# Kernel optimization log

Measured on AMD Instinct MI355X. Metric: run time of the kernel, lower is better.

The kernel has to match this reference:

```python
import jax, jax.numpy as jnp
import numpy as np

N = 100000   # nodes
E = 3200000  # edges
D = 256      # node_dim
H = 64       # hidden (conv1 out)
L = 64       # latent_dim
G = 128      # graphs in batch


def _gcn_conv(x, src, dst, W, b):
    """PyG GCNConv with edge_weight=1: add self-loops, sym deg-norm, scatter-add."""
    n = x.shape[0]
    loop = jnp.arange(n)
    s = jnp.concatenate([src, loop])
    d = jnp.concatenate([dst, loop])
    w = jnp.ones(s.shape[0], x.dtype)
    deg = jax.ops.segment_sum(w, d, num_segments=n)
    dinv = jnp.where(deg > 0, jax.lax.rsqrt(deg), 0.0)
    norm = dinv[s] * w * dinv[d]                      # [E+N]
    h = x @ W                                         # lin (no bias)
    out = jax.ops.segment_sum(h[s] * norm[:, None], d, num_segments=n)
    return out + b


def _mean_pool(z, batch, num_graphs):
    zsum = jax.ops.segment_sum(z, batch, num_segments=num_graphs)
    cnt = jax.ops.segment_sum(jnp.ones(z.shape[0], z.dtype), batch, num_segments=num_graphs)
    return zsum / jnp.clip(cnt, 1.0)[:, None]


def setup_inputs() -> dict:
    key = jax.random.key(0)
    ks = jax.random.split(key, 8)
    x = jax.random.normal(ks[0], (N, D), jnp.float32)
    edge_index = jax.random.randint(ks[1], (2, E), 0, N, dtype=jnp.int64)
    batch = jnp.sort(jax.random.randint(ks[2], (N,), 0, G, dtype=jnp.int64))
    glorot = lambda k, fi, fo: jax.random.normal(k, (fi, fo), jnp.float32) / np.sqrt(fi).astype(np.float32)
    return {
        "x": x, "edge_index": edge_index, "batch": batch,
        "W1": glorot(ks[3], D, H), "b1": jnp.zeros((H,), jnp.float32),
        "W2": glorot(ks[4], H, L), "b2": jnp.zeros((L,), jnp.float32),
        "Wd1": glorot(ks[5], L, 64), "bd1": jnp.zeros((64,), jnp.float32),
        "Wd2": glorot(ks[6], 64, D), "bd2": jnp.zeros((D,), jnp.float32),
    }


def reference(x, edge_index, batch, W1, b1, W2, b2, Wd1, bd1, Wd2, bd2):
    src, dst = edge_index[0], edge_index[1]
    h = jax.nn.relu(_gcn_conv(x, src, dst, W1, b1))
    z = _gcn_conv(h, src, dst, W2, b2)
    z_pool = _mean_pool(z, batch, G)                  # [G, L]
    x_hat = jax.nn.relu(z_pool @ Wd1 + bd1) @ Wd2 + bd2  # [G, D]
    return (x_hat, z_pool)
```

## Files before the change

kernel.cpp:

```cpp
#include <hip/hip_runtime.h>
#include <hip/hip_bf16.h>
#include <hip/hip_fp16.h>
#include <hip/hip_fp8.h>

namespace {
constexpr int kN = 100000;
constexpr int kE = 3200000;
constexpr int kD = 256;
constexpr int kH = 64;
constexpr int kG = 128;

constexpr int kNB   = 782;
constexpr int kCapS = 4608;
constexpr int kCap  = 64;
constexpr int kNPad = 100352;

constexpr size_t kSlBytes = (size_t)(kN + 1) * 32;

constexpr size_t kAlign = 512;
constexpr size_t align_up(size_t v) { return (v + kAlign - 1) & ~(kAlign - 1); }

constexpr size_t OFF_CURD = 0;
constexpr size_t OFF_GCNT = OFF_CURD + align_up(kNB * 4);
constexpr size_t OFF_QRAW = OFF_GCNT + kAlign;
constexpr size_t ZERO_BYTES = OFF_QRAW + align_up((size_t)kG * kH * 4);
constexpr size_t OFF_CNT  = ZERO_BYTES;
constexpr size_t OFF_DINV = OFF_CNT + align_up((size_t)kNPad * 4);
constexpr size_t OFF_SD   = OFF_DINV + align_up((size_t)kNPad * 4);
constexpr size_t OFF_REC  = OFF_SD + align_up((size_t)kNB * kCapS * 4);
constexpr size_t OFF_HL   = OFF_REC + align_up((size_t)kNPad * kCap * 4);
constexpr size_t OFF_H2   = OFF_HL + align_up((size_t)(kN + 1) * kH);
}

__device__ __forceinline__ unsigned pack4_fp8(float a, float b, float c, float d) {
#if __has_builtin(__builtin_amdgcn_cvt_pk_fp8_f32)
    int r = 0;
    r = __builtin_amdgcn_cvt_pk_fp8_f32(a, b, r, false);
    r = __builtin_amdgcn_cvt_pk_fp8_f32(c, d, r, true);
    return (unsigned)r;
#else
    __hip_fp8_e4m3 qa(a), qb(b), qc(c), qd(d);
    return (unsigned)qa.__x | ((unsigned)qb.__x << 8)
         | ((unsigned)qc.__x << 16) | ((unsigned)qd.__x << 24);
#endif
}

__device__ __forceinline__ void add4q(float (&acc)[4], unsigned u) {
#if __has_builtin(__builtin_amdgcn_cvt_pk_f32_fp8)
    typedef float v2f __attribute__((ext_vector_type(2)));
    v2f f0 = __builtin_amdgcn_cvt_pk_f32_fp8((int)u, false);
    v2f f1 = __builtin_amdgcn_cvt_pk_f32_fp8((int)u, true);
    acc[0] += f0.x; acc[1] += f0.y; acc[2] += f1.x; acc[3] += f1.y;
#else
    #pragma unroll
    for (int j = 0; j < 4; ++j) {
        __hip_fp8_e4m3 v; v.__x = (__hip_fp8_storage_t)((u >> (8 * j)) & 0xFF);
        acc[j] += (float)v;
    }
#endif
}

__device__ __forceinline__ void add8q(float (&acc)[8], uint2 u) {
    float* a0 = acc;
    float* a1 = acc + 4;
    add4q(*(float(*)[4])a0, u.x);
    add4q(*(float(*)[4])a1, u.y);
}

__global__ __launch_bounds__(1024) void k_bucket(const int* __restrict__ src,
                                                 const int* __restrict__ dst,
                                                 int* __restrict__ curD,
                                                 unsigned* __restrict__ streamD) {
    __shared__ int cD[kNB], bD[kNB];
    int t = threadIdx.x;
    for (int i = t; i < kNB; i += 1024) cD[i] = 0;
    __syncthreads();
    int e0 = blockIdx.x * 16384;
    #pragma unroll
    for (int k = 0; k < 16; ++k) {
        int e = e0 + k * 1024 + t;
        if (e < kE) atomicAdd(&cD[dst[e] >> 7], 1);
    }
    __syncthreads();
    for (int i = t; i < kNB; i += 1024)
        bD[i] = cD[i] ? atomicAdd(&curD[i], cD[i]) : 0;
    __syncthreads();
    for (int i = t; i < kNB; i += 1024) cD[i] = 0;
    __syncthreads();
    #pragma unroll
    for (int k = 0; k < 16; ++k) {
        int e = e0 + k * 1024 + t;
        if (e < kE) {
            int s = src[e], d = dst[e];
            int pd = bD[d >> 7] + atomicAdd(&cD[d >> 7], 1);
            if (pd < kCapS)
                streamD[(size_t)(d >> 7) * kCapS + pd] =
                    ((unsigned)(d & 127) << 17) | (unsigned)s;
        }
    }
}

__global__ __launch_bounds__(256) void k_fillB(const int* __restrict__ curD,
                                               const unsigned* __restrict__ streamD,
                                               int* __restrict__ rec,
                                               int* __restrict__ cnt) {
    __shared__ int lc[128];
    int b = blockIdx.x, t = threadIdx.x;
    if (t < 128) lc[t] = 0;
    __syncthreads();
    int n = min(curD[b], kCapS);
    const unsigned* sp = streamD + (size_t)b * kCapS;
    for (int i = t; i < n; i += 256) {
        unsigned u = sp[i];
        int dlo = (u >> 17) & 127;
        int slot = atomicAdd(&lc[dlo], 1);
        if (slot < kCap)
            rec[((((size_t)b << 7) | dlo) << 6) + slot] = (int)(u & 0x1FFFF);
    }
    __syncthreads();
    if (t < 128) {
        int d = (b << 7) + t;
        if (d < kNPad) cnt[d] = lc[t];
    }
}

__global__ void k_gcnt(const int* __restrict__ batch, int* __restrict__ gcnt) {
    __shared__ int h[kG];
    int t = threadIdx.x;
    if (t < kG) h[t] = 0;
    __syncthreads();
    for (int i = blockIdx.x * blockDim.x + t; i < kN; i += gridDim.x * blockDim.x)
        atomicAdd(&h[batch[i]], 1);
    __syncthreads();
    if (t < kG && h[t]) atomicAdd(&gcnt[t], h[t]);
}

__global__ void k_dinv(const int* __restrict__ cnt, float* __restrict__ dinv,
                       unsigned* __restrict__ hl8, unsigned* __restrict__ h8) {
    int i = blockIdx.x * blockDim.x + threadIdx.x;
    if (i < kN) dinv[i] = rsqrtf((float)(cnt[i] + 1));
    if (blockIdx.x == 0 && threadIdx.x < 32) {
        int t = threadIdx.x;
        if (t < 16) {
            hl8[(size_t)kN * 16 + t] = 0u;
        } else {
            int s = (t >> 3) & 1;
            int j = t & 7;
            h8[(s * kSlBytes) / 4 + (size_t)kN * 8 + j] = 0u;
        }
    }
}

__global__ __launch_bounds__(256) void k_gemm1(const float* __restrict__ x,
                                               const float* __restrict__ W1,
                                               const float* __restrict__ dinv,
                                               unsigned char* __restrict__ hl8) {
    constexpr int TM = 64;
    constexpr int KC = 32;
    __shared__ float xs[KC][TM + 4];
    __shared__ float ws[KC][kH];
    int t = threadIdx.x;
    int tx = t & 15;
    int ty = t >> 4;
    int nb = blockIdx.x * TM;
    float acc[4][4] = {};
    for (int k0 = 0; k0 < kD; k0 += KC) {
        #pragma unroll
        for (int j = 0; j < 2; ++j) {
            int id = t * 2 + j;
            int row = id >> 3;
            int c4 = (id & 7) * 4;
            int node = nb + row;
            if (node >= kN) node = kN - 1;
            float4 v = *(const float4*)(x + (size_t)node * kD + k0 + c4);
            xs[c4 + 0][row] = v.x;
            xs[c4 + 1][row] = v.y;
            xs[c4 + 2][row] = v.z;
            xs[c4 + 3][row] = v.w;
        }
        #pragma unroll
        for (int j = 0; j < 2; ++j) {
            int id = t * 2 + j;
            int row = id >> 4;
            int c4 = (id & 15) * 4;
            float4 v = *(const float4*)(W1 + (size_t)(k0 + row) * kH + c4);
            *(float4*)&ws[row][c4] = v;
        }
        __syncthreads();
        #pragma unroll
        for (int kk = 0; kk < KC; ++kk) {
            float4 a = *(const float4*)&xs[kk][ty * 4];
            float4 b = *(const float4*)&ws[kk][tx * 4];
            acc[0][0] = fmaf(a.x, b.x, acc[0][0]); acc[0][1] = fmaf(a.x, b.y, acc[0][1]);
            acc[0][2] = fmaf(a.x, b.z, acc[0][2]); acc[0][3] = fmaf(a.x, b.w, acc[0][3]);
            acc[1][0] = fmaf(a.y, b.x, acc[1][0]); acc[1][1] = fmaf(a.y, b.y, acc[1][1]);
            acc[1][2] = fmaf(a.y, b.z, acc[1][2]); acc[1][3] = fmaf(a.y, b.w, acc[1][3]);
            acc[2][0] = fmaf(a.z, b.x, acc[2][0]); acc[2][1] = fmaf(a.z, b.y, acc[2][1]);
            acc[2][2] = fmaf(a.z, b.z, acc[2][2]); acc[2][3] = fmaf(a.z, b.w, acc[2][3]);
            acc[3][0] = fmaf(a.w, b.x, acc[3][0]); acc[3][1] = fmaf(a.w, b.y, acc[3][1]);
            acc[3][2] = fmaf(a.w, b.z, acc[3][2]); acc[3][3] = fmaf(a.w, b.w, acc[3][3]);
        }
        __syncthreads();
    }
    #pragma unroll
    for (int i = 0; i < 4; ++i) {
        int node = nb + ty * 4 + i;
        if (node < kN) {
            float di = dinv[node];
            unsigned p = pack4_fp8(di * acc[i][0], di * acc[i][1],
                                   di * acc[i][2], di * acc[i][3]);
            *(unsigned*)(hl8 + (size_t)node * kH + tx * 4) = p;
        }
    }
}

__global__ __launch_bounds__(256) void k_conv1(const int* __restrict__ rec,
                                               const int* __restrict__ cnt,
                                               const float* __restrict__ dinv,
                                               const unsigned char* __restrict__ hl8,
                                               const float* __restrict__ b1,
                                               unsigned char* __restrict__ h8) {
    int tid = threadIdx.x;
    int lane = tid & 63;
    int node = blockIdx.x * 4 + (tid >> 6);
    if (node >= kN) return;
    int slot = lane >> 3;
    int fl = lane & 7;
    size_t base = (size_t)node << 6;
    int len = min(cnt[node], kCap);
    float acc0[8] = {}, acc1[8] = {};
    for (int c0 = 0; c0 < len; c0 += 16) {
        int e0 = c0 + slot;
        int e1 = c0 + 8 + slot;
        int s0 = (e0 < len) ? rec[base + e0] : kN;
        int s1 = (e1 < len) ? rec[base + e1] : kN;
        uint2 v0 = *(const uint2*)(hl8 + ((size_t)s0 << 6) + fl * 8);
        uint2 v1 = *(const uint2*)(hl8 + ((size_t)s1 << 6) + fl * 8);
        add8q(acc0, v0);
        add8q(acc1, v1);
    }
    #pragma unroll
    for (int j = 0; j < 8; ++j) acc0[j] += acc1[j];
    #pragma unroll
    for (int d = 8; d < 64; d <<= 1) {
        #pragma unroll
        for (int j = 0; j < 8; ++j) acc0[j] += __shfl_xor(acc0[j], d, 64);
    }
    if (slot == 0) {
        uint2 sv = *(const uint2*)(hl8 + ((size_t)node << 6) + fl * 8);
        add8q(acc0, sv);
        float di = dinv[node];
        float4 ba = *(const float4*)(b1 + fl * 8);
        float4 bb = *(const float4*)(b1 + fl * 8 + 4);
        float bz[8] = {ba.x, ba.y, ba.z, ba.w, bb.x, bb.y, bb.z, bb.w};
        float r[8];
        #pragma unroll
        for (int j = 0; j < 8; ++j)
            r[j] = di * fmaxf(fmaf(di, acc0[j], bz[j]), 0.f);
        uint2 o;
        o.x = pack4_fp8(r[0], r[1], r[2], r[3]);
        o.y = pack4_fp8(r[4], r[5], r[6], r[7]);
        *(uint2*)(h8 + (size_t)(fl >> 2) * kSlBytes + (size_t)node * 32 + (fl & 3) * 8) = o;
    }
}

__global__ __launch_bounds__(256) void k_pool3(const int* __restrict__ rec,
                                               const int* __restrict__ cnt,
                                               const float* __restrict__ dinv,
                                               const unsigned char* __restrict__ h8,
                                               const int* __restrict__ batch,
                                               float* __restrict__ q_raw) {
    constexpr int CHUNK = 8;
    int tid = threadIdx.x;
    int lane = tid & 63;
    int slice = blockIdx.x & 1;
    int wid = (blockIdx.x >> 1) * 4 + (tid >> 6);
    int n0 = wid * CHUNK;
    if (n0 >= kN) return;
    int n1 = n0 + CHUNK; if (n1 > kN) n1 = kN;
    int slot = lane >> 3;
    int fl = lane & 7;
    const unsigned char* hsl = h8 + slice * kSlBytes;
    float racc[4] = {};
    int gcur = batch[n0];
    for (int i = n0; i < n1; ++i) {
        int g = batch[i];
        if (g != gcur) {
            #pragma unroll
            for (int d = 8; d < 64; d <<= 1) {
                #pragma unroll
                for (int j = 0; j < 4; ++j) racc[j] += __shfl_xor(racc[j], d, 64);
            }
            if (lane < 8) {
                #pragma unroll
                for (int j = 0; j < 4; ++j)
                    atomicAdd(&q_raw[(gcur << 6) + slice * 32 + fl * 4 + j], racc[j]);
            }
            #pragma unroll
            for (int j = 0; j < 4; ++j) racc[j] = 0.f;
            gcur = g;
        }
        size_t base = (size_t)i << 6;
        int len = min(cnt[i], kCap);
        float ns0[4] = {}, ns1[4] = {};
        for (int c0 = 0; c0 < len; c0 += 16) {
            int e0 = c0 + slot;
            int e1 = c0 + 8 + slot;
            int s0 = (e0 < len) ? rec[base + e0] : kN;
            int s1 = (e1 < len) ? rec[base + e1] : kN;
            unsigned v0 = *(const unsigned*)(hsl + (size_t)s0 * 32 + fl * 4);
            unsigned v1 = *(const unsigned*)(hsl + (size_t)s1 * 32 + fl * 4);
            add4q(ns0, v0);
            add4q(ns1, v1);
        }
        if (slot == 0) {
            unsigned sv = *(const unsigned*)(hsl + (size_t)i * 32 + fl * 4);
            add4q(ns0, sv);
        }
        float di = dinv[i];
        #pragma unroll
        for (int j = 0; j < 4; ++j) racc[j] = fmaf(di, ns0[j] + ns1[j], racc[j]);
    }
    #pragma unroll
    for (int d = 8; d < 64; d <<= 1) {
        #pragma unroll
        for (int j = 0; j < 4; ++j) racc[j] += __shfl_xor(racc[j], d, 64);
    }
    if (lane < 8) {
        #pragma unroll
        for (int j = 0; j < 4; ++j)
            atomicAdd(&q_raw[(gcur << 6) + slice * 32 + fl * 4 + j], racc[j]);
    }
}

__global__ __launch_bounds__(64) void k_head(const float* __restrict__ q_raw,
                                             const int* __restrict__ gcnt,
                                             const float* __restrict__ W2,
                                             const float* __restrict__ b2,
                                             const float* __restrict__ Wd1,
                                             const float* __restrict__ bd1,
                                             const float* __restrict__ Wd2,
                                             const float* __restrict__ bd2,
                                             float* __restrict__ out) {
    __shared__ float zm[kH], zp[kH], tt[kH];
    int g = blockIdx.x, c = threadIdx.x;
    int cg = gcnt[g];
    float inv = (cg > 0) ? 1.f / (float)cg : 0.f;
    zm[c] = q_raw[(size_t)g * kH + c] * inv;
    __syncthreads();
    float a = b2[c];
    #pragma unroll 8
    for (int k = 0; k < kH; ++k) a = fmaf(zm[k], W2[k * kH + c], a);
    if (cg == 0) a = 0.f;
    out[(size_t)kG * kD + (size_t)g * kH + c] = a;
    zp[c] = a;
    __syncthreads();
    float t = bd1[c];
    #pragma unroll 8
    for (int k = 0; k < kH; ++k) t = fmaf(zp[k], Wd1[k * 64 + c], t);
    tt[c] = fmaxf(t, 0.f);
    __syncthreads();
    #pragma unroll
    for (int j4 = 0; j4 < 4; ++j4) {
        int col = c + j4 * 64;
        float v = bd2[col];
        #pragma unroll 8
        for (int k = 0; k < 64; ++k) v = fmaf(tt[k], Wd2[k * kD + col], v);
        out[(size_t)g * kD + col] = v;
    }
}

extern "C" void kernel_launch(void* const* d_in, const int* in_sizes, int n_in,
                              void* d_out, int out_size, void* d_ws, size_t ws_size,
                              hipStream_t stream) {
    const float* x    = (const float*)d_in[0];
    const int*   ei   = (const int*)d_in[1];
    const int*   src  = ei;
    const int*   dst  = ei + kE;
    const int*   batch= (const int*)d_in[2];
    const float* W1   = (const float*)d_in[3];
    const float* b1   = (const float*)d_in[4];
    const float* W2   = (const float*)d_in[5];
    const float* b2   = (const float*)d_in[6];
    const float* Wd1  = (const float*)d_in[7];
    const float* bd1  = (const float*)d_in[8];
    const float* Wd2  = (const float*)d_in[9];
    const float* bd2  = (const float*)d_in[10];
    float* out = (float*)d_out;

    char* ws = (char*)d_ws;
    int*           curD  = (int*)(ws + OFF_CURD);
    int*           gcnt  = (int*)(ws + OFF_GCNT);
    float*         q_raw = (float*)(ws + OFF_QRAW);
    int*           cnt   = (int*)(ws + OFF_CNT);
    float*         dinv  = (float*)(ws + OFF_DINV);
    unsigned*      sD    = (unsigned*)(ws + OFF_SD);
    int*           rec   = (int*)(ws + OFF_REC);
    unsigned char* hl8   = (unsigned char*)(ws + OFF_HL);
    unsigned char* h8    = (unsigned char*)(ws + OFF_H2);

    hipMemsetAsync(d_ws, 0, ZERO_BYTES, stream);

    const int nBucketBlocks = (kE + 16383) / 16384;

    k_bucket<<<nBucketBlocks, 1024, 0, stream>>>(src, dst, curD, sD);
    k_fillB<<<kNB, 256, 0, stream>>>(curD, sD, rec, cnt);

    k_gcnt<<<128, 256, 0, stream>>>(batch, gcnt);
    k_dinv<<<(kN + 255) / 256, 256, 0, stream>>>(cnt, dinv,
                                                 (unsigned*)hl8, (unsigned*)h8);

    k_gemm1<<<(kN + 63) / 64, 256, 0, stream>>>(x, W1, dinv, hl8);

    k_conv1<<<(kN + 3) / 4, 256, 0, stream>>>(rec, cnt, dinv, hl8, b1, h8);

    const int nPoolWaves = (kN + 7) / 8;
    k_pool3<<<((nPoolWaves + 3) / 4) * 2, 256, 0, stream>>>(rec, cnt, dinv, h8, batch, q_raw);

    k_head<<<kG, 64, 0, stream>>>(q_raw, gcnt, W2, b2, Wd1, bd1, Wd2, bd2, out);
}
```

Before: 293.6 us.

## Split pool3 gather by source-node halves instead of feature slices

Changes the layer-2 pooling gather to partition work by source-node range (two halves of the node set) rather than by feature halves. Each block now reads full 64-byte fp8 rows from a contiguous row-major h8 buffer, but only for sources in its half, so each block's working set of gathered rows is about half the table. This is meant to improve cache locality for the random gathers. In exchange each block does 8-wide accumulation and atomics, and loads for masked-out sources are redirected to a dummy zero row rather than skipped.

```diff
diff --git a/kernel.cpp b/kernel.cpp
--- a/kernel.cpp
+++ b/kernel.cpp
@@ -9,13 +9,12 @@
 constexpr int kD = 256;
 constexpr int kH = 64;
 constexpr int kG = 128;
+constexpr int kHalf = 50000;
 
 constexpr int kNB   = 782;
 constexpr int kCapS = 4608;
 constexpr int kCap  = 64;
 constexpr int kNPad = 100352;
-
-constexpr size_t kSlBytes = (size_t)(kN + 1) * 32;
 
 constexpr size_t kAlign = 512;
 constexpr size_t align_up(size_t v) { return (v + kAlign - 1) & ~(kAlign - 1); }
@@ -141,13 +140,8 @@
     if (i < kN) dinv[i] = rsqrtf((float)(cnt[i] + 1));
     if (blockIdx.x == 0 && threadIdx.x < 32) {
         int t = threadIdx.x;
-        if (t < 16) {
-            hl8[(size_t)kN * 16 + t] = 0u;
-        } else {
-            int s = (t >> 3) & 1;
-            int j = t & 7;
-            h8[(s * kSlBytes) / 4 + (size_t)kN * 8 + j] = 0u;
-        }
+        unsigned* p = (t < 16) ? hl8 : h8;
+        p[((size_t)kN * kH) / 4 + (t & 15)] = 0u;
     }
 }
 
@@ -260,7 +254,7 @@
         uint2 o;
         o.x = pack4_fp8(r[0], r[1], r[2], r[3]);
         o.y = pack4_fp8(r[4], r[5], r[6], r[7]);
-        *(uint2*)(h8 + (size_t)(fl >> 2) * kSlBytes + (size_t)node * 32 + (fl & 3) * 8) = o;
+        *(uint2*)(h8 + ((size_t)node << 6) + fl * 8) = o;
     }
 }
 
@@ -273,15 +267,14 @@
     constexpr int CHUNK = 8;
     int tid = threadIdx.x;
     int lane = tid & 63;
-    int slice = blockIdx.x & 1;
+    int half = blockIdx.x & 1;
     int wid = (blockIdx.x >> 1) * 4 + (tid >> 6);
     int n0 = wid * CHUNK;
     if (n0 >= kN) return;
     int n1 = n0 + CHUNK; if (n1 > kN) n1 = kN;
     int slot = lane >> 3;
     int fl = lane & 7;
-    const unsigned char* hsl = h8 + slice * kSlBytes;
-    float racc[4] = {};
+    float racc[8] = {};
     int gcur = batch[n0];
     for (int i = n0; i < n1; ++i) {
         int g = batch[i];
@@ -289,47 +282,49 @@
             #pragma unroll
             for (int d = 8; d < 64; d <<= 1) {
                 #pragma unroll
-                for (int j = 0; j < 4; ++j) racc[j] += __shfl_xor(racc[j], d, 64);
+                for (int j = 0; j < 8; ++j) racc[j] += __shfl_xor(racc[j], d, 64);
             }
             if (lane < 8) {
                 #pragma unroll
-                for (int j = 0; j < 4; ++j)
-                    atomicAdd(&q_raw[(gcur << 6) + slice * 32 + fl * 4 + j], racc[j]);
+                for (int j = 0; j < 8; ++j)
+                    atomicAdd(&q_raw[(gcur << 6) + fl * 8 + j], racc[j]);
             }
             #pragma unroll
-            for (int j = 0; j < 4; ++j) racc[j] = 0.f;
+            for (int j = 0; j < 8; ++j) racc[j] = 0.f;
             gcur = g;
         }
         size_t base = (size_t)i << 6;
         int len = min(cnt[i], kCap);
-        float ns0[4] = {}, ns1[4] = {};
+        float ns0[8] = {}, ns1[8] = {};
         for (int c0 = 0; c0 < len; c0 += 16) {
             int e0 = c0 + slot;
             int e1 = c0 + 8 + slot;
             int s0 = (e0 < len) ? rec[base + e0] : kN;
             int s1 = (e1 < len) ? rec[base + e1] : kN;
-            unsigned v0 = *(const unsigned*)(hsl + (size_t)s0 * 32 + fl * 4);
-            unsigned v1 = *(const unsigned*)(hsl + (size_t)s1 * 32 + fl * 4);
-            add4q(ns0, v0);
-            add4q(ns1, v1);
-        }
-        if (slot == 0) {
-            unsigned sv = *(const unsigned*)(hsl + (size_t)i * 32 + fl * 4);
-            add4q(ns0, sv);
+            s0 = (((s0 >= kHalf) ? 1 : 0) == half) ? s0 : kN;
+            s1 = (((s1 >= kHalf) ? 1 : 0) == half) ? s1 : kN;
+            uint2 v0 = *(const uint2*)(h8 + ((size_t)s0 << 6) + fl * 8);
+            uint2 v1 = *(const uint2*)(h8 + ((size_t)s1 << 6) + fl * 8);
+            add8q(ns0, v0);
+            add8q(ns1, v1);
+        }
+        if (slot == 0 && (((i >= kHalf) ? 1 : 0) == half)) {
+            uint2 sv = *(const uint2*)(h8 + ((size_t)i << 6) + fl * 8);
+            add8q(ns0, sv);
         }
         float di = dinv[i];
         #pragma unroll
-        for (int j = 0; j < 4; ++j) racc[j] = fmaf(di, ns0[j] + ns1[j], racc[j]);
+        for (int j = 0; j < 8; ++j) racc[j] = fmaf(di, ns0[j] + ns1[j], racc[j]);
     }
     #pragma unroll
     for (int d = 8; d < 64; d <<= 1) {
         #pragma unroll
-        for (int j = 0; j < 4; ++j) racc[j] += __shfl_xor(racc[j], d, 64);
+        for (int j = 0; j < 8; ++j) racc[j] += __shfl_xor(racc[j], d, 64);
     }
     if (lane < 8) {
         #pragma unroll
-        for (int j = 0; j < 4; ++j)
-            atomicAdd(&q_raw[(gcur << 6) + slice * 32 + fl * 4 + j], racc[j]);
+        for (int j = 0; j < 8; ++j)
+            atomicAdd(&q_raw[(gcur << 6) + fl * 8 + j], racc[j]);
     }
 }
 
```

New measurement: 385.1 us. 1.31x slower.
